# Performance work log

Measured on AMD Instinct MI355X. Metric: run time of the kernel, lower is better.

## Reference

```python
import jax, jax.numpy as jnp
import numpy as np

B, T, F = 65536, 79, 8
C = 256        # RNN channels
DW = 256       # dense width


def setup_inputs() -> dict:
    key = jax.random.key(0)
    ks = jax.random.split(key, 6)
    s = lambda *d: 1.0 / np.sqrt(d[0])
    x = jax.random.normal(ks[0], (B, T, F), dtype=jnp.float32)
    W = jax.random.normal(ks[1], (F, C), dtype=jnp.float32) * s(F)   # input kernel
    U = jax.random.normal(ks[2], (C, C), dtype=jnp.float32) * s(C)   # recurrent kernel
    b = jnp.zeros((C,), dtype=jnp.float32)
    W1 = jax.random.normal(ks[3], (C, DW), dtype=jnp.float32) * s(C)  # MLP dense
    b1 = jnp.zeros((DW,), dtype=jnp.float32)
    return {"x": x, "W": W, "U": U, "b": b, "W1": W1, "b1": b1}


def reference(x, W, U, b, W1, b1):
    # SimpleRNN(relu, go_backwards=True): iterate over reversed z dim,
    # h_t = relu(x_t @ W + h_{t-1} @ U + b); return final state.
    xr = jnp.flip(x, axis=1)                     # go_backwards over dim 1
    xs = jnp.transpose(xr, (1, 0, 2))            # (T, B, F) for scan
    h0 = jnp.zeros((x.shape[0], U.shape[0]), dtype=x.dtype)

    def step(h, xt):
        h = jax.nn.relu(xt @ W + h @ U + b)
        return h, None

    h_last, _ = jax.lax.scan(step, h0, xs)       # (B, C)
    # MLPBlock with depth=1: single Dense(DW, relu)
    out = jax.nn.relu(h_last @ W1 + b1)          # (B, DW)
    return out
```

## Files before the change

### kernel.cpp

```cpp
#include <hip/hip_runtime.h>


#define B_ROWS 65536
#define T_STEPS 79
#define F_IN 8
#define C_DIM 256

typedef _Float16 h16;
typedef __attribute__((ext_vector_type(8))) _Float16 half8;
typedef __attribute__((ext_vector_type(16))) float f32x16;
typedef __attribute__((ext_vector_type(4))) float f32x4;

__device__ __forceinline__ void load_bfrags(half8 bf[17],
                                            const float* __restrict__ M,
                                            const float* __restrict__ Wx,
                                            const float* __restrict__ bias,
                                            int n, int q) {
  #pragma unroll
  for (int kf = 0; kf < 16; ++kf) {
    const int k0 = 16 * kf + 8 * q;
    half8 v;
    #pragma unroll
    for (int j = 0; j < 8; ++j)
      v[j] = (h16)M[(size_t)(k0 + j) * C_DIM + n];
    bf[kf] = v;
  }
  half8 v;
  #pragma unroll
  for (int j = 0; j < 8; ++j) v[j] = (h16)0.f;
  if (q == 0) {
    if (Wx) {
      #pragma unroll
      for (int j = 0; j < 8; ++j) v[j] = (h16)Wx[j * C_DIM + n];
    }
  } else {
    v[0] = (h16)bias[n];
  }
  bf[16] = v;
}


#define LOAD_X(lo, hi)                                                      \
  f32x4 lo[2], hi[2];                                                       \
  if (q == 0) {                                                             \
    _Pragma("unroll") for (int mf = 0; mf < 2; ++mf) {                      \
      const f32x4* xp = (const f32x4*)(xbase + xoff[mf]);                   \
      lo[mf] = xp[0];                                                       \
      hi[mf] = xp[1];                                                       \
      xoff[mf] -= F_IN * 4;                                                 \
    }                                                                       \
  }

#define MAKE_XA(xa, lo, hi)                                                 \
  half8 xa[2];                                                              \
  _Pragma("unroll") for (int mf = 0; mf < 2; ++mf) {                        \
    if (q == 0) {                                                           \
      half8 v;                                                              \
      v[0] = (h16)lo[mf][0]; v[1] = (h16)lo[mf][1];                         \
      v[2] = (h16)lo[mf][2]; v[3] = (h16)lo[mf][3];                         \
      v[4] = (h16)hi[mf][0]; v[5] = (h16)hi[mf][1];                         \
      v[6] = (h16)hi[mf][2]; v[7] = (h16)hi[mf][3];                         \
      xa[mf] = v;                                                           \
    } else {                                                                \
      half8 v;                                                              \
      _Pragma("unroll") for (int j = 0; j < 8; ++j) v[j] = (h16)0.f;        \
      v[0] = (h16)1.f;                  \
      xa[mf] = v;                                                           \
    }                                                                       \
  }

#define EPILOGUE(acc0, acc1, WB)                                            \
  _Pragma("unroll") for (int g = 0; g < 16; ++g) {                          \
    const int rr_g = (g & 3) + ((g >> 2) << 3);                             \
    const int Kg = (rr_g << 9) | (rr_g << 4);                               \
    char* const wp = lds + (wbase ^ Kg);                                    \
    *(h16*)(wp + (WB) * 32768) = (h16)fmaxf(acc0[g], 0.f);                  \
    *(h16*)(wp + (WB) * 32768 + 16384) = (h16)fmaxf(acc1[g], 0.f);          \
  }

#define STEP(RBUF)                                                          \
  do {                                                                      \
    LOAD_X(lo_, hi_);                                                       \
    __syncthreads();       \
    MAKE_XA(xa_, lo_, hi_);                                                 \
    f32x16 acc0_ = __builtin_amdgcn_mfma_f32_32x32x16_f16(                  \
        xa_[0], bf[16], (f32x16)(0.f), 0, 0, 0);                            \
    f32x16 acc1_ = __builtin_amdgcn_mfma_f32_32x32x16_f16(                  \
        xa_[1], bf[16], (f32x16)(0.f), 0, 0, 0);                            \
    _Pragma("unroll") for (int kf = 0; kf < 16; ++kf) {                     \
      const char* const rp = lds + (rbase ^ (kf << 5));                     \
      const half8 a0_ = *(const half8*)(rp + (RBUF)*32768);                 \
      acc0_ = __builtin_amdgcn_mfma_f32_32x32x16_f16(a0_, bf[kf], acc0_,    \
                                                     0, 0, 0);              \
      const half8 a1_ = *(const half8*)(rp + (RBUF)*32768 + 16384);         \
      acc1_ = __builtin_amdgcn_mfma_f32_32x32x16_f16(a1_, bf[kf], acc1_,    \
                                                     0, 0, 0);              \
    }                                                                       \
    EPILOGUE(acc0_, acc1_, (RBUF) ^ 1);                                     \
  } while (0)

__global__ __launch_bounds__(512)
__attribute__((amdgpu_waves_per_eu(2, 2)))
void rnn_fused(const float* __restrict__ x, const float* __restrict__ W,
               const float* __restrict__ U, const float* __restrict__ b,
               const float* __restrict__ W1, const float* __restrict__ b1,
               float* __restrict__ out) {
  __shared__ alignas(16) h16 hbuf[2][64 * 256];

  const int tid = threadIdx.x;
  const int lane = tid & 63;
  const int wave = tid >> 6;
  const int l31 = lane & 31;
  const int q = lane >> 5;
  const int row0 = blockIdx.x << 6;
  const int n = (wave << 5) + l31;

  half8 bf[17];
  load_bfrags(bf, U, W, b, n, q);

  char* const lds = (char*)hbuf;

  const int rbase = (l31 << 9) ^ (q << 4) ^ (l31 << 4);
  const int wbase = (q << 11) ^ (q << 6) ^ ((n >> 3) << 4) ^ ((n & 7) << 1);

  const char* const xbase = (const char*)x;
  int xoff[2];
  #pragma unroll
  for (int mf = 0; mf < 2; ++mf)
    xoff[mf] = ((row0 + (mf << 5) + l31) * (T_STEPS * F_IN) +
                (T_STEPS - 1) * F_IN)
               << 2;

  {
    LOAD_X(lo_, hi_);
    MAKE_XA(xa_, lo_, hi_);
    f32x16 acc0_ = __builtin_amdgcn_mfma_f32_32x32x16_f16(
        xa_[0], bf[16], (f32x16)(0.f), 0, 0, 0);
    f32x16 acc1_ = __builtin_amdgcn_mfma_f32_32x32x16_f16(
        xa_[1], bf[16], (f32x16)(0.f), 0, 0, 0);
    EPILOGUE(acc0_, acc1_, 1);
  }

  #pragma unroll 1
  for (int sp = 0; sp < (T_STEPS - 1) / 2; ++sp) {
    STEP(1);
    STEP(0);
  }

  load_bfrags(bf, W1, nullptr, b1, n, q);
  half8 xaf;
  #pragma unroll
  for (int j = 0; j < 8; ++j) xaf[j] = (h16)0.f;
  if (q == 1) xaf[0] = (h16)1.f;

  f32x16 acc0 = __builtin_amdgcn_mfma_f32_32x32x16_f16(
      xaf, bf[16], (f32x16)(0.f), 0, 0, 0);
  f32x16 acc1 = __builtin_amdgcn_mfma_f32_32x32x16_f16(
      xaf, bf[16], (f32x16)(0.f), 0, 0, 0);

  __syncthreads();

  #pragma unroll
  for (int kf = 0; kf < 16; ++kf) {
    const char* const rp = lds + (rbase ^ (kf << 5));
    const half8 a0 = *(const half8*)(rp + 32768);
    acc0 = __builtin_amdgcn_mfma_f32_32x32x16_f16(a0, bf[kf], acc0, 0, 0, 0);
    const half8 a1 = *(const half8*)(rp + 32768 + 16384);
    acc1 = __builtin_amdgcn_mfma_f32_32x32x16_f16(a1, bf[kf], acc1, 0, 0, 0);
  }

  #pragma unroll
  for (int g = 0; g < 16; ++g) {
    const int rr = (g & 3) + ((g >> 2) << 3) + (q << 2);
    out[(size_t)(row0 + rr) * C_DIM + n] = fmaxf(acc0[g], 0.f);
    out[(size_t)(row0 + 32 + rr) * C_DIM + n] = fmaxf(acc1[g], 0.f);
  }
}

extern "C" void kernel_launch(void* const* d_in, const int* in_sizes, int n_in,
                              void* d_out, int out_size, void* d_ws,
                              size_t ws_size, hipStream_t stream) {
  const float* x  = (const float*)d_in[0];
  const float* W  = (const float*)d_in[1];
  const float* U  = (const float*)d_in[2];
  const float* b  = (const float*)d_in[3];
  const float* W1 = (const float*)d_in[4];
  const float* b1 = (const float*)d_in[5];
  float* out = (float*)d_out;

  rnn_fused<<<B_ROWS / 64, 512, 0, stream>>>(x, W, U, b, W1, b1, out);
}
```

Baseline: 818.6 us.

## Give each wave two 32-column tiles, halving block size to 256 threads

Each wave now computes 64 output columns (two N-fragments) instead of 32, so each A fragment read from LDS feeds two MFMAs. Block size drops from 512 to 256 threads per 64-row tile. This halves LDS read traffic per MFMA and gives barriers fewer waves to synchronise. The cost is twice the register-resident B fragments and accumulators per wave, which risks spills or lower occupancy while waves_per_eu stays fixed at 2.

```diff
diff --git a/kernel.cpp b/kernel.cpp
--- a/kernel.cpp
+++ b/kernel.cpp
@@ -11,32 +11,36 @@
 typedef __attribute__((ext_vector_type(16))) float f32x16;
 typedef __attribute__((ext_vector_type(4))) float f32x4;
 
-__device__ __forceinline__ void load_bfrags(half8 bf[17],
+__device__ __forceinline__ void load_bfrags(half8 bf[2][17],
                                             const float* __restrict__ M,
                                             const float* __restrict__ Wx,
                                             const float* __restrict__ bias,
-                                            int n, int q) {
-  #pragma unroll
-  for (int kf = 0; kf < 16; ++kf) {
-    const int k0 = 16 * kf + 8 * q;
+                                            int ncol0, int q) {
+  #pragma unroll
+  for (int nf = 0; nf < 2; ++nf) {
+    const int n = ncol0 + 32 * nf;
+    #pragma unroll
+    for (int kf = 0; kf < 16; ++kf) {
+      const int k0 = 16 * kf + 8 * q;
+      half8 v;
+      #pragma unroll
+      for (int j = 0; j < 8; ++j)
+        v[j] = (h16)M[(size_t)(k0 + j) * C_DIM + n];
+      bf[nf][kf] = v;
+    }
     half8 v;
     #pragma unroll
-    for (int j = 0; j < 8; ++j)
-      v[j] = (h16)M[(size_t)(k0 + j) * C_DIM + n];
-    bf[kf] = v;
-  }
-  half8 v;
-  #pragma unroll
-  for (int j = 0; j < 8; ++j) v[j] = (h16)0.f;
-  if (q == 0) {
-    if (Wx) {
-      #pragma unroll
-      for (int j = 0; j < 8; ++j) v[j] = (h16)Wx[j * C_DIM + n];
+    for (int j = 0; j < 8; ++j) v[j] = (h16)0.f;
+    if (q == 0) {
+      if (Wx) {
+        #pragma unroll
+        for (int j = 0; j < 8; ++j) v[j] = (h16)Wx[j * C_DIM + n];
+      }
+    } else {
+      v[0] = (h16)bias[n];
     }
-  } else {
-    v[0] = (h16)bias[n];
-  }
-  bf[16] = v;
+    bf[nf][16] = v;
+  }
 }
 
 
@@ -64,18 +68,21 @@
     } else {                                                                \
       half8 v;                                                              \
       _Pragma("unroll") for (int j = 0; j < 8; ++j) v[j] = (h16)0.f;        \
-      v[0] = (h16)1.f;                  \
+      v[0] = (h16)1.f;                                    \
       xa[mf] = v;                                                           \
     }                                                                       \
   }
 
-#define EPILOGUE(acc0, acc1, WB)                                            \
+#define EPILOGUE(a00, a01, a10, a11, WB)                                    \
   _Pragma("unroll") for (int g = 0; g < 16; ++g) {                          \
     const int rr_g = (g & 3) + ((g >> 2) << 3);                             \
     const int Kg = (rr_g << 9) | (rr_g << 4);                               \
-    char* const wp = lds + (wbase ^ Kg);                                    \
-    *(h16*)(wp + (WB) * 32768) = (h16)fmaxf(acc0[g], 0.f);                  \
-    *(h16*)(wp + (WB) * 32768 + 16384) = (h16)fmaxf(acc1[g], 0.f);          \
+    char* const wp0 = lds + (wb0 ^ Kg);                                     \
+    char* const wp1 = lds + (wb1 ^ Kg);                                     \
+    *(h16*)(wp0 + (WB) * 32768) = (h16)fmaxf(a00[g], 0.f);                  \
+    *(h16*)(wp0 + (WB) * 32768 + 16384) = (h16)fmaxf(a10[g], 0.f);          \
+    *(h16*)(wp1 + (WB) * 32768) = (h16)fmaxf(a01[g], 0.f);                  \
+    *(h16*)(wp1 + (WB) * 32768 + 16384) = (h16)fmaxf(a11[g], 0.f);          \
   }
 
 #define STEP(RBUF)                                                          \
@@ -83,23 +90,31 @@
     LOAD_X(lo_, hi_);                                                       \
     __syncthreads();       \
     MAKE_XA(xa_, lo_, hi_);                                                 \
-    f32x16 acc0_ = __builtin_amdgcn_mfma_f32_32x32x16_f16(                  \
-        xa_[0], bf[16], (f32x16)(0.f), 0, 0, 0);                            \
-    f32x16 acc1_ = __builtin_amdgcn_mfma_f32_32x32x16_f16(                  \
-        xa_[1], bf[16], (f32x16)(0.f), 0, 0, 0);                            \
+    f32x16 a00_ = __builtin_amdgcn_mfma_f32_32x32x16_f16(                   \
+        xa_[0], bf[0][16], (f32x16)(0.f), 0, 0, 0);                         \
+    f32x16 a01_ = __builtin_amdgcn_mfma_f32_32x32x16_f16(                   \
+        xa_[0], bf[1][16], (f32x16)(0.f), 0, 0, 0);                         \
+    f32x16 a10_ = __builtin_amdgcn_mfma_f32_32x32x16_f16(                   \
+        xa_[1], bf[0][16], (f32x16)(0.f), 0, 0, 0);                         \
+    f32x16 a11_ = __builtin_amdgcn_mfma_f32_32x32x16_f16(                   \
+        xa_[1], bf[1][16], (f32x16)(0.f), 0, 0, 0);                         \
     _Pragma("unroll") for (int kf = 0; kf < 16; ++kf) {                     \
       const char* const rp = lds + (rbase ^ (kf << 5));                     \
-      const half8 a0_ = *(const half8*)(rp + (RBUF)*32768);                 \
-      acc0_ = __builtin_amdgcn_mfma_f32_32x32x16_f16(a0_, bf[kf], acc0_,    \
-                                                     0, 0, 0);              \
-      const half8 a1_ = *(const half8*)(rp + (RBUF)*32768 + 16384);         \
-      acc1_ = __builtin_amdgcn_mfma_f32_32x32x16_f16(a1_, bf[kf], acc1_,    \
-                                                     0, 0, 0);              \
+      const half8 f0_ = *(const half8*)(rp + (RBUF)*32768);                 \
+      a00_ = __builtin_amdgcn_mfma_f32_32x32x16_f16(f0_, bf[0][kf], a00_,   \
+                                                    0, 0, 0);               \
+      a01_ = __builtin_amdgcn_mfma_f32_32x32x16_f16(f0_, bf[1][kf], a01_,   \
+                                                    0, 0, 0);               \
+      const half8 f1_ = *(const half8*)(rp + (RBUF)*32768 + 16384);         \
+      a10_ = __builtin_amdgcn_mfma_f32_32x32x16_f16(f1_, bf[0][kf], a10_,   \
+                                                    0, 0, 0);               \
+      a11_ = __builtin_amdgcn_mfma_f32_32x32x16_f16(f1_, bf[1][kf], a11_,   \
+                                                    0, 0, 0);               \
     }                                                                       \
-    EPILOGUE(acc0_, acc1_, (RBUF) ^ 1);                                     \
+    EPILOGUE(a00_, a01_, a10_, a11_, (RBUF) ^ 1);                           \
   } while (0)
 
-__global__ __launch_bounds__(512)
+__global__ __launch_bounds__(256)
 __attribute__((amdgpu_waves_per_eu(2, 2)))
 void rnn_fused(const float* __restrict__ x, const float* __restrict__ W,
                const float* __restrict__ U, const float* __restrict__ b,
@@ -113,15 +128,18 @@
   const int l31 = lane & 31;
   const int q = lane >> 5;
   const int row0 = blockIdx.x << 6;
-  const int n = (wave << 5) + l31;
-
-  half8 bf[17];
-  load_bfrags(bf, U, W, b, n, q);
+  const int ncol0 = (wave << 6) + l31;
+
+  half8 bf[2][17];
+  load_bfrags(bf, U, W, b, ncol0, q);
 
   char* const lds = (char*)hbuf;
 
   const int rbase = (l31 << 9) ^ (q << 4) ^ (l31 << 4);
-  const int wbase = (q << 11) ^ (q << 6) ^ ((n >> 3) << 4) ^ ((n & 7) << 1);
+  const int wb0 = (q << 11) ^ (q << 6) ^ ((ncol0 >> 3) << 4) ^
+                  ((ncol0 & 7) << 1);
+  const int wb1 = (q << 11) ^ (q << 6) ^ (((ncol0 + 32) >> 3) << 4) ^
+                  ((ncol0 & 7) << 1);
 
   const char* const xbase = (const char*)x;
   int xoff[2];
@@ -134,11 +152,15 @@
   {
     LOAD_X(lo_, hi_);
     MAKE_XA(xa_, lo_, hi_);
-    f32x16 acc0_ = __builtin_amdgcn_mfma_f32_32x32x16_f16(
-        xa_[0], bf[16], (f32x16)(0.f), 0, 0, 0);
-    f32x16 acc1_ = __builtin_amdgcn_mfma_f32_32x32x16_f16(
-        xa_[1], bf[16], (f32x16)(0.f), 0, 0, 0);
-    EPILOGUE(acc0_, acc1_, 1);
+    f32x16 a00_ = __builtin_amdgcn_mfma_f32_32x32x16_f16(
+        xa_[0], bf[0][16], (f32x16)(0.f), 0, 0, 0);
+    f32x16 a01_ = __builtin_amdgcn_mfma_f32_32x32x16_f16(
+        xa_[0], bf[1][16], (f32x16)(0.f), 0, 0, 0);
+    f32x16 a10_ = __builtin_amdgcn_mfma_f32_32x32x16_f16(
+        xa_[1], bf[0][16], (f32x16)(0.f), 0, 0, 0);
+    f32x16 a11_ = __builtin_amdgcn_mfma_f32_32x32x16_f16(
+        xa_[1], bf[1][16], (f32x16)(0.f), 0, 0, 0);
+    EPILOGUE(a00_, a01_, a10_, a11_, 1);
   }
 
   #pragma unroll 1
@@ -147,33 +169,41 @@
     STEP(0);
   }
 
-  load_bfrags(bf, W1, nullptr, b1, n, q);
+  load_bfrags(bf, W1, nullptr, b1, ncol0, q);
   half8 xaf;
   #pragma unroll
   for (int j = 0; j < 8; ++j) xaf[j] = (h16)0.f;
   if (q == 1) xaf[0] = (h16)1.f;
 
-  f32x16 acc0 = __builtin_amdgcn_mfma_f32_32x32x16_f16(
-      xaf, bf[16], (f32x16)(0.f), 0, 0, 0);
-  f32x16 acc1 = __builtin_amdgcn_mfma_f32_32x32x16_f16(
-      xaf, bf[16], (f32x16)(0.f), 0, 0, 0);
+  f32x16 a00 = __builtin_amdgcn_mfma_f32_32x32x16_f16(
+      xaf, bf[0][16], (f32x16)(0.f), 0, 0, 0);
+  f32x16 a01 = __builtin_amdgcn_mfma_f32_32x32x16_f16(
+      xaf, bf[1][16], (f32x16)(0.f), 0, 0, 0);
+  f32x16 a10 = __builtin_amdgcn_mfma_f32_32x32x16_f16(
+      xaf, bf[0][16], (f32x16)(0.f), 0, 0, 0);
+  f32x16 a11 = __builtin_amdgcn_mfma_f32_32x32x16_f16(
+      xaf, bf[1][16], (f32x16)(0.f), 0, 0, 0);
 
   __syncthreads();
 
   #pragma unroll
   for (int kf = 0; kf < 16; ++kf) {
     const char* const rp = lds + (rbase ^ (kf << 5));
-    const half8 a0 = *(const half8*)(rp + 32768);
-    acc0 = __builtin_amdgcn_mfma_f32_32x32x16_f16(a0, bf[kf], acc0, 0, 0, 0);
-    const half8 a1 = *(const half8*)(rp + 32768 + 16384);
-    acc1 = __builtin_amdgcn_mfma_f32_32x32x16_f16(a1, bf[kf], acc1, 0, 0, 0);
+    const half8 f0 = *(const half8*)(rp + 32768);
+    a00 = __builtin_amdgcn_mfma_f32_32x32x16_f16(f0, bf[0][kf], a00, 0, 0, 0);
+    a01 = __builtin_amdgcn_mfma_f32_32x32x16_f16(f0, bf[1][kf], a01, 0, 0, 0);
+    const half8 f1 = *(const half8*)(rp + 32768 + 16384);
+    a10 = __builtin_amdgcn_mfma_f32_32x32x16_f16(f1, bf[0][kf], a10, 0, 0, 0);
+    a11 = __builtin_amdgcn_mfma_f32_32x32x16_f16(f1, bf[1][kf], a11, 0, 0, 0);
   }
 
   #pragma unroll
   for (int g = 0; g < 16; ++g) {
     const int rr = (g & 3) + ((g >> 2) << 3) + (q << 2);
-    out[(size_t)(row0 + rr) * C_DIM + n] = fmaxf(acc0[g], 0.f);
-    out[(size_t)(row0 + 32 + rr) * C_DIM + n] = fmaxf(acc1[g], 0.f);
+    out[(size_t)(row0 + rr) * C_DIM + ncol0] = fmaxf(a00[g], 0.f);
+    out[(size_t)(row0 + rr) * C_DIM + ncol0 + 32] = fmaxf(a01[g], 0.f);
+    out[(size_t)(row0 + 32 + rr) * C_DIM + ncol0] = fmaxf(a10[g], 0.f);
+    out[(size_t)(row0 + 32 + rr) * C_DIM + ncol0 + 32] = fmaxf(a11[g], 0.f);
   }
 }
 
@@ -188,5 +218,5 @@
   const float* b1 = (const float*)d_in[5];
   float* out = (float*)d_out;
 
-  rnn_fused<<<B_ROWS / 64, 512, 0, stream>>>(x, W, U, b, W1, b1, out);
+  rnn_fused<<<B_ROWS / 64, 256, 0, stream>>>(x, W, U, b, W1, b1, out);
 }
```

After: 1.305 ms. +59.4%, slower.

## Process two independent 64-row groups per block to interleave recurrent chains

Applied to the files above, without the earlier changes.

Each block now handles 128 batch rows as two independent 64-row groups (A and B), each with its own double-buffered hidden state in LDS (128 KB total). Within every time step, group B's x load and MFMA chain follow group A's with a single barrier per step. The aim is to halve the number of barriers per unit of work and to let the two independent chains hide each other's LDS and MFMA latencies. In exchange LDS use doubles, which limits blocks per CU, and the grid is halved to 512 blocks.

```diff
diff --git a/kernel.cpp b/kernel.cpp
--- a/kernel.cpp
+++ b/kernel.cpp
@@ -40,14 +40,14 @@
 }
 
 
-#define LOAD_X(lo, hi)                                                      \
+#define LOAD_X(lo, hi, XOFF)                                                \
   f32x4 lo[2], hi[2];                                                       \
   if (q == 0) {                                                             \
     _Pragma("unroll") for (int mf = 0; mf < 2; ++mf) {                      \
-      const f32x4* xp = (const f32x4*)(xbase + xoff[mf]);                   \
+      const f32x4* xp = (const f32x4*)(xbase + XOFF[mf]);                   \
       lo[mf] = xp[0];                                                       \
       hi[mf] = xp[1];                                                       \
-      xoff[mf] -= F_IN * 4;                                                 \
+      XOFF[mf] -= F_IN * 4;                                                 \
     }                                                                       \
   }
 
@@ -64,39 +64,50 @@
     } else {                                                                \
       half8 v;                                                              \
       _Pragma("unroll") for (int j = 0; j < 8; ++j) v[j] = (h16)0.f;        \
-      v[0] = (h16)1.f;                  \
+      v[0] = (h16)1.f;                                    \
       xa[mf] = v;                                                           \
     }                                                                       \
   }
 
-#define EPILOGUE(acc0, acc1, WB)                                            \
+#define EPILOGUE(acc0, acc1, TB, WB)                                        \
   _Pragma("unroll") for (int g = 0; g < 16; ++g) {                          \
     const int rr_g = (g & 3) + ((g >> 2) << 3);                             \
     const int Kg = (rr_g << 9) | (rr_g << 4);                               \
-    char* const wp = lds + (wbase ^ Kg);                                    \
-    *(h16*)(wp + (WB) * 32768) = (h16)fmaxf(acc0[g], 0.f);                  \
-    *(h16*)(wp + (WB) * 32768 + 16384) = (h16)fmaxf(acc1[g], 0.f);          \
-  }
-
-#define STEP(RBUF)                                                          \
-  do {                                                                      \
-    LOAD_X(lo_, hi_);                                                       \
-    __syncthreads();       \
-    MAKE_XA(xa_, lo_, hi_);                                                 \
-    f32x16 acc0_ = __builtin_amdgcn_mfma_f32_32x32x16_f16(                  \
-        xa_[0], bf[16], (f32x16)(0.f), 0, 0, 0);                            \
-    f32x16 acc1_ = __builtin_amdgcn_mfma_f32_32x32x16_f16(                  \
-        xa_[1], bf[16], (f32x16)(0.f), 0, 0, 0);                            \
-    _Pragma("unroll") for (int kf = 0; kf < 16; ++kf) {                     \
-      const char* const rp = lds + (rbase ^ (kf << 5));                     \
-      const half8 a0_ = *(const half8*)(rp + (RBUF)*32768);                 \
-      acc0_ = __builtin_amdgcn_mfma_f32_32x32x16_f16(a0_, bf[kf], acc0_,    \
-                                                     0, 0, 0);              \
-      const half8 a1_ = *(const half8*)(rp + (RBUF)*32768 + 16384);         \
-      acc1_ = __builtin_amdgcn_mfma_f32_32x32x16_f16(a1_, bf[kf], acc1_,    \
-                                                     0, 0, 0);              \
-    }                                                                       \
-    EPILOGUE(acc0_, acc1_, (RBUF) ^ 1);                                     \
+    char* const wp = lds + (wbase ^ Kg) + (TB) + (WB)*32768;                \
+    *(h16*)(wp) = (h16)fmaxf(acc0[g], 0.f);                                 \
+    *(h16*)(wp + 16384) = (h16)fmaxf(acc1[g], 0.f);                         \
+  }
+
+#define CHAIN(acc0, acc1, TB, RBUF)                                         \
+  _Pragma("unroll") for (int kf = 0; kf < 16; ++kf) {                       \
+    const char* const rp = lds + (rbase ^ (kf << 5)) + (TB) + (RBUF)*32768; \
+    const half8 f0_ = *(const half8*)(rp);                                  \
+    acc0 = __builtin_amdgcn_mfma_f32_32x32x16_f16(f0_, bf[kf], acc0,        \
+                                                  0, 0, 0);                 \
+    const half8 f1_ = *(const half8*)(rp + 16384);                          \
+    acc1 = __builtin_amdgcn_mfma_f32_32x32x16_f16(f1_, bf[kf], acc1,        \
+                                                  0, 0, 0);                 \
+  }
+
+#define STEP(RBUF)                                                         \
+  do {                                                                     \
+    LOAD_X(alo_, ahi_, xoffA);                                             \
+    __syncthreads();    \
+    MAKE_XA(xaA_, alo_, ahi_);                                             \
+    f32x16 aA0_ = __builtin_amdgcn_mfma_f32_32x32x16_f16(                  \
+        xaA_[0], bf[16], (f32x16)(0.f), 0, 0, 0);                          \
+    f32x16 aA1_ = __builtin_amdgcn_mfma_f32_32x32x16_f16(                  \
+        xaA_[1], bf[16], (f32x16)(0.f), 0, 0, 0);                          \
+    LOAD_X(blo_, bhi_, xoffB);           \
+    CHAIN(aA0_, aA1_, 0, RBUF);                                            \
+    EPILOGUE(aA0_, aA1_, 0, (RBUF) ^ 1);      \
+    MAKE_XA(xaB_, blo_, bhi_);                                             \
+    f32x16 aB0_ = __builtin_amdgcn_mfma_f32_32x32x16_f16(                  \
+        xaB_[0], bf[16], (f32x16)(0.f), 0, 0, 0);                          \
+    f32x16 aB1_ = __builtin_amdgcn_mfma_f32_32x32x16_f16(                  \
+        xaB_[1], bf[16], (f32x16)(0.f), 0, 0, 0);                          \
+    CHAIN(aB0_, aB1_, 65536, RBUF);                                        \
+    EPILOGUE(aB0_, aB1_, 65536, (RBUF) ^ 1);                               \
   } while (0)
 
 __global__ __launch_bounds__(512)
@@ -105,14 +116,14 @@
                const float* __restrict__ U, const float* __restrict__ b,
                const float* __restrict__ W1, const float* __restrict__ b1,
                float* __restrict__ out) {
-  __shared__ alignas(16) h16 hbuf[2][64 * 256];
+  __shared__ alignas(16) h16 hbuf[4][64 * 256];
 
   const int tid = threadIdx.x;
   const int lane = tid & 63;
   const int wave = tid >> 6;
   const int l31 = lane & 31;
   const int q = lane >> 5;
-  const int row0 = blockIdx.x << 6;
+  const int row0 = blockIdx.x << 7;
   const int n = (wave << 5) + l31;
 
   half8 bf[17];
@@ -124,21 +135,32 @@
   const int wbase = (q << 11) ^ (q << 6) ^ ((n >> 3) << 4) ^ ((n & 7) << 1);
 
   const char* const xbase = (const char*)x;
-  int xoff[2];
-  #pragma unroll
-  for (int mf = 0; mf < 2; ++mf)
-    xoff[mf] = ((row0 + (mf << 5) + l31) * (T_STEPS * F_IN) +
-                (T_STEPS - 1) * F_IN)
-               << 2;
+  int xoffA[2], xoffB[2];
+  #pragma unroll
+  for (int mf = 0; mf < 2; ++mf) {
+    xoffA[mf] = ((row0 + (mf << 5) + l31) * (T_STEPS * F_IN) +
+                 (T_STEPS - 1) * F_IN)
+                << 2;
+    xoffB[mf] = ((row0 + 64 + (mf << 5) + l31) * (T_STEPS * F_IN) +
+                 (T_STEPS - 1) * F_IN)
+                << 2;
+  }
 
   {
-    LOAD_X(lo_, hi_);
-    MAKE_XA(xa_, lo_, hi_);
-    f32x16 acc0_ = __builtin_amdgcn_mfma_f32_32x32x16_f16(
-        xa_[0], bf[16], (f32x16)(0.f), 0, 0, 0);
-    f32x16 acc1_ = __builtin_amdgcn_mfma_f32_32x32x16_f16(
-        xa_[1], bf[16], (f32x16)(0.f), 0, 0, 0);
-    EPILOGUE(acc0_, acc1_, 1);
+    LOAD_X(alo_, ahi_, xoffA);
+    LOAD_X(blo_, bhi_, xoffB);
+    MAKE_XA(xaA_, alo_, ahi_);
+    f32x16 aA0_ = __builtin_amdgcn_mfma_f32_32x32x16_f16(
+        xaA_[0], bf[16], (f32x16)(0.f), 0, 0, 0);
+    f32x16 aA1_ = __builtin_amdgcn_mfma_f32_32x32x16_f16(
+        xaA_[1], bf[16], (f32x16)(0.f), 0, 0, 0);
+    EPILOGUE(aA0_, aA1_, 0, 1);
+    MAKE_XA(xaB_, blo_, bhi_);
+    f32x16 aB0_ = __builtin_amdgcn_mfma_f32_32x32x16_f16(
+        xaB_[0], bf[16], (f32x16)(0.f), 0, 0, 0);
+    f32x16 aB1_ = __builtin_amdgcn_mfma_f32_32x32x16_f16(
+        xaB_[1], bf[16], (f32x16)(0.f), 0, 0, 0);
+    EPILOGUE(aB0_, aB1_, 65536, 1);
   }
 
   #pragma unroll 1
@@ -153,27 +175,27 @@
   for (int j = 0; j < 8; ++j) xaf[j] = (h16)0.f;
   if (q == 1) xaf[0] = (h16)1.f;
 
-  f32x16 acc0 = __builtin_amdgcn_mfma_f32_32x32x16_f16(
-      xaf, bf[16], (f32x16)(0.f), 0, 0, 0);
-  f32x16 acc1 = __builtin_amdgcn_mfma_f32_32x32x16_f16(
+  f32x16 aA0 = __builtin_amdgcn_mfma_f32_32x32x16_f16(
+      xaf, bf[16], (f32x16)(0.f), 0, 0, 0);
+  f32x16 aA1 = __builtin_amdgcn_mfma_f32_32x32x16_f16(
+      xaf, bf[16], (f32x16)(0.f), 0, 0, 0);
+  f32x16 aB0 = __builtin_amdgcn_mfma_f32_32x32x16_f16(
+      xaf, bf[16], (f32x16)(0.f), 0, 0, 0);
+  f32x16 aB1 = __builtin_amdgcn_mfma_f32_32x32x16_f16(
       xaf, bf[16], (f32x16)(0.f), 0, 0, 0);
 
   __syncthreads();
 
-  #pragma unroll
-  for (int kf = 0; kf < 16; ++kf) {
-    const char* const rp = lds + (rbase ^ (kf << 5));
-    const half8 a0 = *(const half8*)(rp + 32768);
-    acc0 = __builtin_amdgcn_mfma_f32_32x32x16_f16(a0, bf[kf], acc0, 0, 0, 0);
-    const half8 a1 = *(const half8*)(rp + 32768 + 16384);
-    acc1 = __builtin_amdgcn_mfma_f32_32x32x16_f16(a1, bf[kf], acc1, 0, 0, 0);
-  }
+  CHAIN(aA0, aA1, 0, 1);
+  CHAIN(aB0, aB1, 65536, 1);
 
   #pragma unroll
   for (int g = 0; g < 16; ++g) {
     const int rr = (g & 3) + ((g >> 2) << 3) + (q << 2);
-    out[(size_t)(row0 + rr) * C_DIM + n] = fmaxf(acc0[g], 0.f);
-    out[(size_t)(row0 + 32 + rr) * C_DIM + n] = fmaxf(acc1[g], 0.f);
+    out[(size_t)(row0 + rr) * C_DIM + n] = fmaxf(aA0[g], 0.f);
+    out[(size_t)(row0 + 32 + rr) * C_DIM + n] = fmaxf(aA1[g], 0.f);
+    out[(size_t)(row0 + 64 + rr) * C_DIM + n] = fmaxf(aB0[g], 0.f);
+    out[(size_t)(row0 + 96 + rr) * C_DIM + n] = fmaxf(aB1[g], 0.f);
   }
 }
 
@@ -188,5 +210,5 @@
   const float* b1 = (const float*)d_in[5];
   float* out = (float*)d_out;
 
-  rnn_fused<<<B_ROWS / 64, 512, 0, stream>>>(x, W, U, b, W1, b1, out);
+  rnn_fused<<<B_ROWS / 128, 512, 0, stream>>>(x, W, U, b, W1, b1, out);
 }
```

Measured after the change: 913.0 us. 1.12x slower.
